# Kernel tuning notes

Hardware: AMD Instinct MI355X
Metric: run time of the kernel (lower is better)

The kernel has to match this reference:

```python
import jax, jax.numpy as jnp
import numpy as np

INF = 1e10  # stand-in for the original global INF constant
D_MODEL = 1024
N_HEADS = 16
SCALE = float(np.sqrt(D_MODEL))  # Attention is built with full d_key, so scale = sqrt(d_model)


def setup_inputs() -> dict:
    key = jax.random.key(0)
    ks = jax.random.split(key, 8)
    B, S, D = 4, 2048, D_MODEL
    s = 1.0 / np.sqrt(D)
    return {
        "query": jax.random.normal(ks[0], (B, S, D), jnp.float32),
        "key": jax.random.normal(ks[1], (B, S, D), jnp.float32),
        "value": jax.random.normal(ks[2], (B, S, D), jnp.float32),
        "wq": jax.random.normal(ks[3], (D, D), jnp.float32) * s,
        "bq": jnp.zeros((D,), jnp.float32),
        "wk": jax.random.normal(ks[4], (D, D), jnp.float32) * s,
        "bk": jnp.zeros((D,), jnp.float32),
        "wv": jax.random.normal(ks[5], (D, D), jnp.float32) * s,
        "bv": jnp.zeros((D,), jnp.float32),
        "wo": jax.random.normal(ks[6], (D, D), jnp.float32) * s,
        "bo": jnp.zeros((D,), jnp.float32),
    }


def reference(query, key, value, wq, bq, wk, bk, wv, bv, wo, bo):
    B, S, D = query.shape
    H = N_HEADS
    dh = D // H
    q = query @ wq + bq
    k = key @ wk + bk
    v = value @ wv + bv
    # split heads: [B, S, H, dh]
    q = q.reshape(B, S, H, dh)
    k = k.reshape(B, S, H, dh)
    v = v.reshape(B, S, H, dh)
    # raw dot products (unscaled), then causal mask subtracted (as in original),
    # then divide by sqrt(d_key) and softmax
    scores = jnp.einsum("bqhd,bkhd->bhqk", q, k)
    causal = jnp.triu(jnp.ones((S, S), scores.dtype), k=1) * INF
    scores = scores - causal  # broadcast over [B, H]
    attn = jax.nn.softmax(scores / SCALE, axis=-1)
    out = jnp.einsum("bhqk,bkhd->bqhd", attn, v).reshape(B, S, D)
    return out @ wo + bo
```

## Files before the change

kernel.cpp:

```cpp
#include <hip/hip_runtime.h>
#include <hip/hip_bf16.h>

typedef __bf16 bf16_t;
typedef __bf16 bf16x8 __attribute__((ext_vector_type(8)));
typedef float f32x4 __attribute__((ext_vector_type(4)));

#define MFMA16(a, b, c) __builtin_amdgcn_mfma_f32_16x16x32_bf16((a), (b), (c), 0, 0, 0)

static constexpr int S_LEN = 2048;
static constexpr int DM = 1024;
static constexpr int NH = 16;
static constexpr int DH = 64;

typedef const __attribute__((address_space(1))) unsigned int gu32;
typedef __attribute__((address_space(3))) unsigned int lu32;
__device__ __forceinline__ void gl_lds16(const void* src, void* dst) {
    __builtin_amdgcn_global_load_lds((gu32*)src, (lu32*)dst, 16, 0, 0);
}

struct PreArgs { const float* w[4]; bf16_t* o[4]; const float* s[3]; bf16_t* d[3]; };

__global__ __launch_bounds__(256) void pre_kernel(PreArgs p) {
    int bid = blockIdx.x;
    int tid = threadIdx.x;
    if (bid < 1024) {
        int wi = bid >> 8;
        int tb = bid & 255;
        int k0 = (tb >> 4) * 64;
        int n0 = (tb & 15) * 64;
        const float* w = p.w[wi];
        bf16_t* o = p.o[wi];
        __shared__ bf16_t t[64 * 66];
#pragma unroll
        for (int i = 0; i < 4; ++i) {
            int f = tid + 256 * i;
            int row = f >> 4;
            int c4 = f & 15;
            f32x4 v = *reinterpret_cast<const f32x4*>(w + (size_t)(k0 + row) * DM + n0 + c4 * 4);
            int base = row * 66 + c4 * 4;
            t[base + 0] = (bf16_t)v[0];
            t[base + 1] = (bf16_t)v[1];
            t[base + 2] = (bf16_t)v[2];
            t[base + 3] = (bf16_t)v[3];
        }
        __syncthreads();
#pragma unroll
        for (int i = 0; i < 2; ++i) {
            int c = tid + 256 * i;
            int n = c >> 3;
            int ck = c & 7;
            union { bf16_t h[8]; uint4 u; } cv;
#pragma unroll
            for (int j = 0; j < 8; ++j) cv.h[j] = t[(ck * 8 + j) * 66 + n];
            *reinterpret_cast<uint4*>(o + (size_t)(n0 + n) * DM + k0 + ck * 8) = cv.u;
        }
    } else {
        int cbid = bid - 1024;
        int ti = cbid >> 12;
        size_t idx = (size_t)(((cbid & 4095) << 8) | tid) * 8;
        const float* s = p.s[ti];
        bf16_t* d = p.d[ti];
        f32x4 v0 = *reinterpret_cast<const f32x4*>(s + idx);
        f32x4 v1 = *reinterpret_cast<const f32x4*>(s + idx + 4);
        union { bf16_t h[8]; uint4 u; } cv;
#pragma unroll
        for (int j = 0; j < 4; ++j) { cv.h[j] = (bf16_t)v0[j]; cv.h[4 + j] = (bf16_t)v1[j]; }
        *reinterpret_cast<uint4*>(d + idx) = cv.u;
    }
}

#define GEMM_CORE(Ab_, BT_)                                                          \
    __shared__ bf16_t a_buf[2][128 * 32];                                            \
    __shared__ bf16_t b_buf[2][128 * 32];                                            \
    f32x4 zero = {0.f, 0.f, 0.f, 0.f};                                               \
    f32x4 acc[4][4];                                                                 \
    _Pragma("unroll") for (int m = 0; m < 4; ++m)                                    \
        _Pragma("unroll") for (int n = 0; n < 4; ++n) acc[m][n] = zero;              \
    int wr = (w >> 1) * 64, wc = (w & 1) * 64;                                       \
    auto stage = [&](int buf, int kt) {                                              \
        int k0 = kt * 32;                                                            \
        _Pragma("unroll") for (int i = 0; i < 2; ++i) {                              \
            int r16 = (w * 2 + i) * 16;                                              \
            int row = r16 + (l >> 2), ch = l & 3;                                    \
            gl_lds16(Ab_ + (size_t)(m0 + row) * 1024 + k0 + ch * 8, &a_buf[buf][r16 * 32]); \
            gl_lds16(BT_ + (size_t)(n0 + row) * 1024 + k0 + ch * 8, &b_buf[buf][r16 * 32]); \
        }                                                                            \
    };                                                                               \
    stage(0, 0);                                                                     \
    int cur = 0;                                                                     \
    for (int kt = 0; kt < 32; ++kt) {                                                \
        __syncthreads();                                                             \
        if (kt + 1 < 32) stage(cur ^ 1, kt + 1);                                     \
        bf16x8 af[4], bfr[4];                                                        \
        _Pragma("unroll") for (int m = 0; m < 4; ++m)                                \
            af[m] = *reinterpret_cast<bf16x8*>(&a_buf[cur][(wr + m * 16 + lc) * 32 + g * 8]); \
        _Pragma("unroll") for (int n = 0; n < 4; ++n)                                \
            bfr[n] = *reinterpret_cast<bf16x8*>(&b_buf[cur][(wc + n * 16 + lc) * 32 + g * 8]); \
        _Pragma("unroll") for (int m = 0; m < 4; ++m)                                \
            _Pragma("unroll") for (int n = 0; n < 4; ++n)                            \
                acc[m][n] = MFMA16(af[m], bfr[n], acc[m][n]);                        \
        cur ^= 1;                                                                    \
    }

struct QKVArgs {
    const bf16_t* A[3]; const bf16_t* BT[3]; const float* bias[3];
    bf16_t* out[3]; float alpha0;
};

__global__ __launch_bounds__(256) void gemm_qkv(QKVArgs a) {
    constexpr int K = 1024, NT = 32;
    int bid = blockIdx.x;
    int wi = bid >> 10;
    int sub = bid & 1023;
    int bm = (sub & 7) * 8 + ((sub >> 3) & 7);
    int bn = sub >> 6;
    int tid = threadIdx.x;
    int w = tid >> 6, l = tid & 63;
    int g = l >> 4, lc = l & 15;

    const bf16_t* Ab = a.A[wi];
    const bf16_t* BT = a.BT[wi];

    __shared__ bf16_t a_s[3][128 * 32];
    __shared__ bf16_t b_s[3][64 * 32];

    f32x4 zero = {0.f, 0.f, 0.f, 0.f};
    f32x4 acc[4][2];
#pragma unroll
    for (int m = 0; m < 4; ++m)
#pragma unroll
        for (int n = 0; n < 2; ++n) acc[m][n] = zero;

    int m0 = bm * 128, n0 = bn * 64;
    int wr = (w >> 1) * 64, wc = (w & 1) * 32;

    auto stage = [&](int buf, int kt) {
        int k0 = kt * 32;
#pragma unroll
        for (int i = 0; i < 2; ++i) {
            int r16 = (w * 2 + i) * 16;
            int row = r16 + (l >> 2), ch = l & 3;
            gl_lds16(Ab + (size_t)(m0 + row) * K + k0 + ch * 8, &a_s[buf][r16 * 32]);
        }
        int r16 = w * 16;
        int row = r16 + (l >> 2), ch = l & 3;
        gl_lds16(BT + (size_t)(n0 + row) * K + k0 + ch * 8, &b_s[buf][r16 * 32]);
    };

    stage(0, 0);
    stage(1, 1);
    int rd = 0;
    for (int kt = 0; kt < NT; ++kt) {
        if (kt < NT - 1) asm volatile("s_waitcnt vmcnt(3)" ::: "memory");
        else             asm volatile("s_waitcnt vmcnt(0)" ::: "memory");
        __builtin_amdgcn_s_barrier();
        asm volatile("" ::: "memory");
        if (kt + 2 < NT) {
            int wb = rd + 2; if (wb >= 3) wb -= 3;
            stage(wb, kt + 2);
        }
        bf16x8 af[4], bfr[2];
#pragma unroll
        for (int m = 0; m < 4; ++m)
            af[m] = *reinterpret_cast<bf16x8*>(&a_s[rd][(wr + m * 16 + lc) * 32 + g * 8]);
#pragma unroll
        for (int n = 0; n < 2; ++n)
            bfr[n] = *reinterpret_cast<bf16x8*>(&b_s[rd][(wc + n * 16 + lc) * 32 + g * 8]);
#pragma unroll
        for (int m = 0; m < 4; ++m)
#pragma unroll
            for (int n = 0; n < 2; ++n)
                acc[m][n] = MFMA16(af[m], bfr[n], acc[m][n]);
        if (++rd == 3) rd = 0;
    }

    float alpha = (wi == 0) ? a.alpha0 : 1.0f;
    const float* bias = a.bias[wi];
    bf16_t* Cp = a.out[wi];
    if (wi == 2) {
#pragma unroll
        for (int n = 0; n < 2; ++n) {
            int ng = n0 + wc + n * 16 + lc;
            float bv = bias[ng];
            int h = ng >> 6, d = ng & 63;
#pragma unroll
            for (int m = 0; m < 4; ++m) {
                int s0g = m0 + wr + m * 16 + g * 4;
                int b = s0g >> 11, s0 = s0g & 2047;
                union { bf16_t hh[4]; uint2 u; } pk;
#pragma unroll
                for (int r = 0; r < 4; ++r)
                    pk.hh[r] = (bf16_t)(acc[m][n][r] + bv);
                *reinterpret_cast<uint2*>(
                    &Cp[(((size_t)(b * NH + h)) * DH + d) * S_LEN + s0]) = pk.u;
            }
        }
    } else {
#pragma unroll
        for (int n = 0; n < 2; ++n) {
            int ng = n0 + wc + n * 16 + lc;
            float bv = bias[ng];
            int h = ng >> 6, d = ng & 63;
#pragma unroll
            for (int m = 0; m < 4; ++m) {
#pragma unroll
                for (int r = 0; r < 4; ++r) {
                    int mg = m0 + wr + m * 16 + g * 4 + r;
                    int b = mg >> 11, s = mg & 2047;
                    Cp[(((size_t)(b * NH + h)) * S_LEN + s) * DH + d] =
                        (bf16_t)((acc[m][n][r] + bv) * alpha);
                }
            }
        }
    }
}

template <int MODE>
__global__ __launch_bounds__(256) void gemm_k(const bf16_t* __restrict__ Ab,
                                              const bf16_t* __restrict__ BT,
                                              const float* __restrict__ bias,
                                              bf16_t* __restrict__ Cp, float alpha) {
    int bid = blockIdx.x;
    int bm = (bid & 7) * 8 + ((bid >> 3) & 7);
    int bn = bid >> 6;
    int tid = threadIdx.x;
    int w = tid >> 6, l = tid & 63;
    int g = l >> 4, lc = l & 15;
    int m0 = bm * 128, n0 = bn * 128;
    GEMM_CORE(Ab, BT)

    if constexpr (MODE == 2) {
#pragma unroll
        for (int n = 0; n < 4; ++n) {
            int ng = n0 + wc + n * 16 + lc;
            float bv = bias[ng];
            int h = ng >> 6, d = ng & 63;
#pragma unroll
            for (int m = 0; m < 4; ++m) {
                int s0g = m0 + wr + m * 16 + g * 4;
                int b = s0g >> 11, s0 = s0g & 2047;
                union { bf16_t hh[4]; uint2 u; } pk;
#pragma unroll
                for (int r = 0; r < 4; ++r)
                    pk.hh[r] = (bf16_t)((acc[m][n][r] + bv) * alpha);
                *reinterpret_cast<uint2*>(
                    &Cp[(((size_t)(b * NH + h)) * DH + d) * S_LEN + s0]) = pk.u;
            }
        }
    } else {
#pragma unroll
        for (int n = 0; n < 4; ++n) {
            int ng = n0 + wc + n * 16 + lc;
            float bv = bias[ng];
            int h = ng >> 6, d = ng & 63;
#pragma unroll
            for (int m = 0; m < 4; ++m) {
#pragma unroll
                for (int r = 0; r < 4; ++r) {
                    int mg = m0 + wr + m * 16 + g * 4 + r;
                    int b = mg >> 11, s = mg & 2047;
                    Cp[(((size_t)(b * NH + h)) * S_LEN + s) * DH + d] =
                        (bf16_t)((acc[m][n][r] + bv) * alpha);
                }
            }
        }
    }
}

__global__ __launch_bounds__(256) void gemm_o(const bf16_t* __restrict__ Ab,
                                              const bf16_t* __restrict__ BT,
                                              const float* __restrict__ bias,
                                              float* __restrict__ Cp) {
    constexpr int K = 1024, N = 1024;
    int bid = blockIdx.x;
    int bm = (bid & 7) * 8 + ((bid >> 3) & 7);
    int bn = bid >> 6;
    int tid = threadIdx.x;
    int w = tid >> 6, l = tid & 63;
    int g = l >> 4, lc = l & 15;

    __shared__ bf16_t a_buf[2][128 * 32];
    __shared__ bf16_t b_buf[2][64 * 32];

    f32x4 zero = {0.f, 0.f, 0.f, 0.f};
    f32x4 acc[4][2];
#pragma unroll
    for (int m = 0; m < 4; ++m)
#pragma unroll
        for (int n = 0; n < 2; ++n) acc[m][n] = zero;

    int m0 = bm * 128, n0 = bn * 64;
    int wr = (w >> 1) * 64, wc = (w & 1) * 32;

    auto stage = [&](int buf, int kt) {
        int k0 = kt * 32;
#pragma unroll
        for (int i = 0; i < 2; ++i) {
            int r16 = (w * 2 + i) * 16;
            int row = r16 + (l >> 2), ch = l & 3;
            gl_lds16(Ab + (size_t)(m0 + row) * K + k0 + ch * 8, &a_buf[buf][r16 * 32]);
        }
        int r16 = w * 16;
        int row = r16 + (l >> 2), ch = l & 3;
        gl_lds16(BT + (size_t)(n0 + row) * K + k0 + ch * 8, &b_buf[buf][r16 * 32]);
    };

    stage(0, 0);
    int cur = 0;
    for (int kt = 0; kt < K / 32; ++kt) {
        __syncthreads();
        if (kt + 1 < K / 32) stage(cur ^ 1, kt + 1);
        bf16x8 af[4], bfr[2];
#pragma unroll
        for (int m = 0; m < 4; ++m)
            af[m] = *reinterpret_cast<bf16x8*>(&a_buf[cur][(wr + m * 16 + lc) * 32 + g * 8]);
#pragma unroll
        for (int n = 0; n < 2; ++n)
            bfr[n] = *reinterpret_cast<bf16x8*>(&b_buf[cur][(wc + n * 16 + lc) * 32 + g * 8]);
#pragma unroll
        for (int m = 0; m < 4; ++m)
#pragma unroll
            for (int n = 0; n < 2; ++n)
                acc[m][n] = MFMA16(af[m], bfr[n], acc[m][n]);
        cur ^= 1;
    }

#pragma unroll
    for (int n = 0; n < 2; ++n) {
        int ng = n0 + wc + n * 16 + lc;
        float bv = bias[ng];
#pragma unroll
        for (int m = 0; m < 4; ++m) {
#pragma unroll
            for (int r = 0; r < 4; ++r) {
                int mg = m0 + wr + m * 16 + g * 4 + r;
                Cp[(size_t)mg * N + ng] = acc[m][n][r] + bv;
            }
        }
    }
}

__global__ __launch_bounds__(256) void attn_kernel(const bf16_t* __restrict__ Qh,
                                                   const bf16_t* __restrict__ Kh,
                                                   const bf16_t* __restrict__ Vt,
                                                   bf16_t* __restrict__ AO) {
    int bid = blockIdx.x;
    int qt = 31 - (bid >> 6);
    int bh = bid & 63;
    int h = bh & 15;
    int b = bh >> 4;
    int tid = threadIdx.x;
    int w = tid >> 6, l = tid & 63;
    int g = l >> 4, lc = l & 15;
    int q0 = qt * 64 + w * 16;
    int q = q0 + lc;

    __shared__ bf16_t k_lds[2][64 * 64];
    __shared__ bf16_t v_lds[2][64 * 64];
    __shared__ bf16_t p_lds[4][16 * 64];

    size_t head_off = ((size_t)(b * NH + h)) * S_LEN * DH;

    bf16x8 qf[2];
    {
        const bf16_t* qp = Qh + head_off + (size_t)(q0 + lc) * DH + g * 8;
        qf[0] = *reinterpret_cast<const bf16x8*>(qp);
        qf[1] = *reinterpret_cast<const bf16x8*>(qp + 32);
    }

    const bf16_t* kg0; const bf16_t* kg1; const bf16_t* vg0; const bf16_t* vg1;
    int r8a = w * 16, r8b = w * 16 + 8;
    {
        const bf16_t* Kp = Kh + head_off;
        const bf16_t* Vp = Vt + head_off;
        int rowa = r8a + (l >> 3), rowb = r8b + (l >> 3);
        int sca = (l & 7) ^ (rowa & 7), scb = (l & 7) ^ (rowb & 7);
        kg0 = Kp + (size_t)rowa * DH + sca * 8;
        kg1 = Kp + (size_t)rowb * DH + scb * 8;
        vg0 = Vp + (size_t)rowa * S_LEN + sca * 8;
        vg1 = Vp + (size_t)rowb * S_LEN + scb * 8;
    }

    f32x4 zero = {0.f, 0.f, 0.f, 0.f};
    f32x4 o_acc[4];
#pragma unroll
    for (int nt = 0; nt < 4; ++nt) o_acc[nt] = zero;
    float l_part = 0.f;

    int sw = lc & 7;

    auto stageKV = [&](int buf) {
        gl_lds16(kg0, &k_lds[buf][r8a * 64]);
        gl_lds16(vg0, &v_lds[buf][r8a * 64]);
        gl_lds16(kg1, &k_lds[buf][r8b * 64]);
        gl_lds16(vg1, &v_lds[buf][r8b * 64]);
    };

    stageKV(0);
    int cur = 0;
    for (int t = 0; t <= qt; ++t) {
        int kv0 = t * 64;
        __syncthreads();
        if (t < qt) {
            kg0 += 64 * DH; kg1 += 64 * DH; vg0 += 64; vg1 += 64;
            stageKV(cur ^ 1);
        }

        f32x4 sc[4];
#pragma unroll
        for (int nt = 0; nt < 4; ++nt) {
            int row = nt * 16 + lc;
            bf16x8 kf0 = *reinterpret_cast<bf16x8*>(&k_lds[cur][row * 64 + ((g) ^ sw) * 8]);
            bf16x8 kf1 = *reinterpret_cast<bf16x8*>(&k_lds[cur][row * 64 + ((4 + g) ^ sw) * 8]);
            f32x4 s = zero;
            s = MFMA16(kf0, qf[0], s);
            s = MFMA16(kf1, qf[1], s);
            sc[nt] = s;
        }
        if (t == qt) {
#pragma unroll
            for (int nt = 0; nt < 4; ++nt)
#pragma unroll
                for (int r = 0; r < 4; ++r) {
                    int kv = kv0 + nt * 16 + g * 4 + r;
                    if (kv > q) sc[nt][r] = -1e30f;
                }
        }
#pragma unroll
        for (int nt = 0; nt < 4; ++nt)
#pragma unroll
            for (int r = 0; r < 4; ++r) sc[nt][r] = exp2f(sc[nt][r]);
#pragma unroll
        for (int nt = 0; nt < 4; ++nt)
            l_part += sc[nt][0] + sc[nt][1] + sc[nt][2] + sc[nt][3];
#pragma unroll
        for (int nt = 0; nt < 4; ++nt) {
            union { bf16_t hh[4]; uint2 u; } pk;
#pragma unroll
            for (int r = 0; r < 4; ++r) pk.hh[r] = (bf16_t)sc[nt][r];
            int cu = nt * 2 + (g >> 1);
            *reinterpret_cast<uint2*>(
                &p_lds[w][lc * 64 + ((cu ^ sw) * 8) + (g & 1) * 4]) = pk.u;
        }
        bf16x8 pf0 = *reinterpret_cast<bf16x8*>(&p_lds[w][lc * 64 + ((g) ^ sw) * 8]);
        bf16x8 pf1 = *reinterpret_cast<bf16x8*>(&p_lds[w][lc * 64 + ((4 + g) ^ sw) * 8]);
#pragma unroll
        for (int nt = 0; nt < 4; ++nt) {
            int row = nt * 16 + lc;
            bf16x8 vf0 = *reinterpret_cast<bf16x8*>(&v_lds[cur][row * 64 + ((g) ^ sw) * 8]);
            bf16x8 vf1 = *reinterpret_cast<bf16x8*>(&v_lds[cur][row * 64 + ((4 + g) ^ sw) * 8]);
            o_acc[nt] = MFMA16(pf0, vf0, o_acc[nt]);
            o_acc[nt] = MFMA16(pf1, vf1, o_acc[nt]);
        }
        cur ^= 1;
    }

    float l_s = l_part;
    l_s += __shfl_xor(l_s, 16, 64);
    l_s += __shfl_xor(l_s, 32, 64);

#pragma unroll
    for (int r = 0; r < 4; ++r) {
        float lr = __shfl(l_s, g * 4 + r, 64);
        float inv = 1.0f / lr;
        int qq = q0 + g * 4 + r;
        size_t base = ((size_t)b * S_LEN + qq) * DM + h * DH;
#pragma unroll
        for (int nt = 0; nt < 4; ++nt)
            AO[base + nt * 16 + lc] = (bf16_t)(o_acc[nt][r] * inv);
    }
}

extern "C" void kernel_launch(void* const* d_in, const int* in_sizes, int n_in,
                              void* d_out, int out_size, void* d_ws, size_t ws_size,
                              hipStream_t stream) {
    (void)in_sizes; (void)n_in; (void)out_size;
    const float* query = (const float*)d_in[0];
    const float* key   = (const float*)d_in[1];
    const float* value = (const float*)d_in[2];
    const float* wq = (const float*)d_in[3];
    const float* bq = (const float*)d_in[4];
    const float* wk = (const float*)d_in[5];
    const float* bk = (const float*)d_in[6];
    const float* wv = (const float*)d_in[7];
    const float* bv = (const float*)d_in[8];
    const float* wo = (const float*)d_in[9];
    const float* bo = (const float*)d_in[10];
    float* out = (float*)d_out;

    char* ws = (char*)d_ws;
    const size_t Mi = (size_t)1 << 20;
    bf16_t* wqT = (bf16_t*)(ws + 0 * Mi);
    bf16_t* wkT = (bf16_t*)(ws + 2 * Mi);
    bf16_t* wvT = (bf16_t*)(ws + 4 * Mi);
    bf16_t* woT = (bf16_t*)(ws + 6 * Mi);
    bf16_t* Qh  = (bf16_t*)(ws + 8 * Mi);
    bf16_t* Kh  = (bf16_t*)(ws + 24 * Mi);
    bf16_t* Vt  = (bf16_t*)(ws + 40 * Mi);
    bf16_t* AO  = (bf16_t*)(ws + 56 * Mi);

    const float QALPHA = 0.04508422f;

    bool roomy = (ws_size >= 120 * Mi);
    bf16_t* Xq;
    bf16_t* Xk;
    bf16_t* Xv;
    if (roomy) {
        Xq = (bf16_t*)(ws + 72 * Mi);
        Xk = (bf16_t*)(ws + 88 * Mi);
        Xv = (bf16_t*)(ws + 104 * Mi);
    } else {
        Xq = (bf16_t*)(ws + 24 * Mi);
        Xk = (bf16_t*)(ws + 40 * Mi);
        Xv = (bf16_t*)(ws + 56 * Mi);
    }

    PreArgs p;
    p.w[0] = wq; p.w[1] = wk; p.w[2] = wv; p.w[3] = wo;
    p.o[0] = wqT; p.o[1] = wkT; p.o[2] = wvT; p.o[3] = woT;
    p.s[0] = query; p.s[1] = key; p.s[2] = value;
    p.d[0] = Xq; p.d[1] = Xk; p.d[2] = Xv;
    pre_kernel<<<dim3(1024 + 3 * 4096), dim3(256), 0, stream>>>(p);

    if (roomy) {
        QKVArgs qa;
        qa.A[0] = Xq; qa.A[1] = Xk; qa.A[2] = Xv;
        qa.BT[0] = wqT; qa.BT[1] = wkT; qa.BT[2] = wvT;
        qa.bias[0] = bq; qa.bias[1] = bk; qa.bias[2] = bv;
        qa.out[0] = Qh; qa.out[1] = Kh; qa.out[2] = Vt;
        qa.alpha0 = QALPHA;
        gemm_qkv<<<dim3(3 * 1024), dim3(256), 0, stream>>>(qa);
    } else {
        gemm_k<0><<<dim3(512), dim3(256), 0, stream>>>(Xq, wqT, bq, Qh, QALPHA);
        gemm_k<0><<<dim3(512), dim3(256), 0, stream>>>(Xk, wkT, bk, Kh, 1.0f);
        gemm_k<2><<<dim3(512), dim3(256), 0, stream>>>(Xv, wvT, bv, Vt, 1.0f);
    }

    attn_kernel<<<dim3(2048), dim3(256), 0, stream>>>(Qh, Kh, Vt, AO);

    gemm_o<<<dim3(1024), dim3(256), 0, stream>>>(AO, woT, bo, out);
}
```

Baseline: 211.3 us.

## Enlarge QKV GEMM tiles to 256x128 with double-buffered LDS pipeline

The fused QKV projection GEMM now uses 256x128 block tiles, so each wave computes a 128x64 sub-tile with 8x4 MFMA accumulators, and the grid shrinks from 3072 to 768 blocks. The triple-buffered async pipeline with explicit vmcnt waits is replaced by a simpler double buffer synchronised with __syncthreads, and the block-swizzled rasterisation is dropped. Larger tiles raise operand reuse per LDS load and cut global traffic. In exchange, register pressure rises and occupancy falls. Load overlap may also be shallower, since the wait at each barrier now drains the next stage's loads.

```diff
diff --git a/kernel.cpp b/kernel.cpp
--- a/kernel.cpp
+++ b/kernel.cpp
@@ -110,10 +110,10 @@
 __global__ __launch_bounds__(256) void gemm_qkv(QKVArgs a) {
     constexpr int K = 1024, NT = 32;
     int bid = blockIdx.x;
-    int wi = bid >> 10;
-    int sub = bid & 1023;
-    int bm = (sub & 7) * 8 + ((sub >> 3) & 7);
-    int bn = sub >> 6;
+    int wi = bid >> 8;
+    int sub = bid & 255;
+    int bm = sub & 31;
+    int bn = sub >> 5;
     int tid = threadIdx.x;
     int w = tid >> 6, l = tid & 63;
     int g = l >> 4, lc = l & 15;
@@ -121,57 +121,52 @@
     const bf16_t* Ab = a.A[wi];
     const bf16_t* BT = a.BT[wi];
 
-    __shared__ bf16_t a_s[3][128 * 32];
-    __shared__ bf16_t b_s[3][64 * 32];
+    __shared__ bf16_t a_s[2][256 * 32];
+    __shared__ bf16_t b_s[2][128 * 32];
 
     f32x4 zero = {0.f, 0.f, 0.f, 0.f};
-    f32x4 acc[4][2];
-#pragma unroll
-    for (int m = 0; m < 4; ++m)
-#pragma unroll
-        for (int n = 0; n < 2; ++n) acc[m][n] = zero;
-
-    int m0 = bm * 128, n0 = bn * 64;
-    int wr = (w >> 1) * 64, wc = (w & 1) * 32;
+    f32x4 acc[8][4];
+#pragma unroll
+    for (int m = 0; m < 8; ++m)
+#pragma unroll
+        for (int n = 0; n < 4; ++n) acc[m][n] = zero;
+
+    int m0 = bm * 256, n0 = bn * 128;
+    int wr = (w >> 1) * 128, wc = (w & 1) * 64;
 
     auto stage = [&](int buf, int kt) {
         int k0 = kt * 32;
+#pragma unroll
+        for (int i = 0; i < 4; ++i) {
+            int r16 = (w * 4 + i) * 16;
+            int row = r16 + (l >> 2), ch = l & 3;
+            gl_lds16(Ab + (size_t)(m0 + row) * K + k0 + ch * 8, &a_s[buf][r16 * 32]);
+        }
 #pragma unroll
         for (int i = 0; i < 2; ++i) {
             int r16 = (w * 2 + i) * 16;
             int row = r16 + (l >> 2), ch = l & 3;
-            gl_lds16(Ab + (size_t)(m0 + row) * K + k0 + ch * 8, &a_s[buf][r16 * 32]);
-        }
-        int r16 = w * 16;
-        int row = r16 + (l >> 2), ch = l & 3;
-        gl_lds16(BT + (size_t)(n0 + row) * K + k0 + ch * 8, &b_s[buf][r16 * 32]);
+            gl_lds16(BT + (size_t)(n0 + row) * K + k0 + ch * 8, &b_s[buf][r16 * 32]);
+        }
     };
 
     stage(0, 0);
-    stage(1, 1);
-    int rd = 0;
+    int cur = 0;
     for (int kt = 0; kt < NT; ++kt) {
-        if (kt < NT - 1) asm volatile("s_waitcnt vmcnt(3)" ::: "memory");
-        else             asm volatile("s_waitcnt vmcnt(0)" ::: "memory");
-        __builtin_amdgcn_s_barrier();
-        asm volatile("" ::: "memory");
-        if (kt + 2 < NT) {
-            int wb = rd + 2; if (wb >= 3) wb -= 3;
-            stage(wb, kt + 2);
-        }
-        bf16x8 af[4], bfr[2];
-#pragma unroll
-        for (int m = 0; m < 4; ++m)
-            af[m] = *reinterpret_cast<bf16x8*>(&a_s[rd][(wr + m * 16 + lc) * 32 + g * 8]);
-#pragma unroll
-        for (int n = 0; n < 2; ++n)
-            bfr[n] = *reinterpret_cast<bf16x8*>(&b_s[rd][(wc + n * 16 + lc) * 32 + g * 8]);
-#pragma unroll
-        for (int m = 0; m < 4; ++m)
-#pragma unroll
-            for (int n = 0; n < 2; ++n)
-                acc[m][n] = MFMA16(af[m], bfr[n], acc[m][n]);
-        if (++rd == 3) rd = 0;
+        __syncthreads();
+        if (kt + 1 < NT) stage(cur ^ 1, kt + 1);
+        bf16x8 bfr[4];
+#pragma unroll
+        for (int n = 0; n < 4; ++n)
+            bfr[n] = *reinterpret_cast<bf16x8*>(&b_s[cur][(wc + n * 16 + lc) * 32 + g * 8]);
+#pragma unroll
+        for (int m = 0; m < 8; ++m) {
+            bf16x8 af = *reinterpret_cast<bf16x8*>(&a_s[cur][(wr + m * 16 + lc) * 32 + g * 8]);
+#pragma unroll
+            for (int n = 0; n < 4; ++n)
+                acc[m][n] = MFMA16(af, bfr[n], acc[m][n]);
+        }
+        cur ^= 1;
     }
 
     float alpha = (wi == 0) ? a.alpha0 : 1.0f;
@@ -179,12 +174,12 @@
     bf16_t* Cp = a.out[wi];
     if (wi == 2) {
 #pragma unroll
-        for (int n = 0; n < 2; ++n) {
+        for (int n = 0; n < 4; ++n) {
             int ng = n0 + wc + n * 16 + lc;
             float bv = bias[ng];
             int h = ng >> 6, d = ng & 63;
 #pragma unroll
-            for (int m = 0; m < 4; ++m) {
+            for (int m = 0; m < 8; ++m) {
                 int s0g = m0 + wr + m * 16 + g * 4;
                 int b = s0g >> 11, s0 = s0g & 2047;
                 union { bf16_t hh[4]; uint2 u; } pk;
@@ -197,12 +192,12 @@
         }
     } else {
 #pragma unroll
-        for (int n = 0; n < 2; ++n) {
+        for (int n = 0; n < 4; ++n) {
             int ng = n0 + wc + n * 16 + lc;
             float bv = bias[ng];
             int h = ng >> 6, d = ng & 63;
 #pragma unroll
-            for (int m = 0; m < 4; ++m) {
+            for (int m = 0; m < 8; ++m) {
 #pragma unroll
                 for (int r = 0; r < 4; ++r) {
                     int mg = m0 + wr + m * 16 + g * 4 + r;
@@ -529,7 +524,7 @@
         qa.bias[0] = bq; qa.bias[1] = bk; qa.bias[2] = bv;
         qa.out[0] = Qh; qa.out[1] = Kh; qa.out[2] = Vt;
         qa.alpha0 = QALPHA;
-        gemm_qkv<<<dim3(3 * 1024), dim3(256), 0, stream>>>(qa);
+        gemm_qkv<<<dim3(3 * 256), dim3(256), 0, stream>>>(qa);
     } else {
         gemm_k<0><<<dim3(512), dim3(256), 0, stream>>>(Xq, wqT, bq, Qh, QALPHA);
         gemm_k<0><<<dim3(512), dim3(256), 0, stream>>>(Xk, wkT, bk, Kh, 1.0f);
```

New measurement: 265.3 us. +25.6%, slower.
